# Optimization experiments

Hardware: AMD Instinct MI355X
Metric: run time of the kernel (lower is better)

The kernel has to match this reference:

```python
import jax, jax.numpy as jnp
import numpy as np

CAM_FL = 540.0
CAM_W, CAM_H = 640, 480
FILTER_STD = 1.0
FILTER_SCALE = 1.0
RADIUS = int(np.ceil(2.0 * FILTER_STD))  # truncate Gaussian footprint at 2 std
K = 2 * RADIUS + 1                        # 5x5 footprint


def setup_inputs() -> dict:
    key = jax.random.key(0)
    k1, k2, k3, k4 = jax.random.split(key, 4)
    B, N = 4, 200000
    locs = jax.random.normal(k1, (B, N, 3), jnp.float32) * 2.0
    camera_pose = jax.random.normal(k2, (B, 3), jnp.float32) * 0.1
    camera_rot = jax.random.normal(k3, (B, 4), jnp.float32)
    # depth in [0, 10): some particles occluded, some visible
    depth_mask = jax.random.uniform(k4, (B, CAM_H, CAM_W), jnp.float32) * 10.0
    return {"locs": locs, "camera_pose": camera_pose,
            "camera_rot": camera_rot, "depth_mask": depth_mask}


def _rot_from_quat(q):
    # Matches torch _rotationMatrixFromQuaternion layout: R[b, i, j]
    qx, qy, qz, qw = q[:, 0], q[:, 1], q[:, 2], q[:, 3]
    qx2, qy2, qz2 = qx * qx, qy * qy, qz * qz
    qxqy, qxqz, qxqw = qx * qy, qx * qz, qx * qw
    qyqz, qyqw, qzqw = qy * qz, qy * qw, qz * qw
    r00 = 1 - 2 * qy2 - 2 * qz2
    r10 = 2 * qxqy - 2 * qzqw
    r20 = 2 * qxqz + 2 * qyqw
    r01 = 2 * qxqy + 2 * qzqw
    r11 = 1 - 2 * qx2 - 2 * qz2
    r21 = 2 * qyqz - 2 * qxqw
    r02 = 2 * qxqz - 2 * qyqw
    r12 = 2 * qyqz + 2 * qxqw
    r22 = 1 - 2 * qx2 - 2 * qy2
    row0 = jnp.stack([r00, r01, r02], axis=-1)
    row1 = jnp.stack([r10, r11, r12], axis=-1)
    row2 = jnp.stack([r20, r21, r22], axis=-1)
    return jnp.stack([row0, row1, row2], axis=-2)  # (B,3,3)


def reference(locs, camera_pose, camera_rot, depth_mask):
    B, N, _ = locs.shape
    # transform into camera frame
    p = locs - camera_pose[:, None, :]
    q = camera_rot / jnp.sqrt(jnp.sum(camera_rot ** 2, axis=1, keepdims=True))
    q = q * jnp.array([-1.0, -1.0, -1.0, 1.0], q.dtype)  # conjugate -> inverse rotation
    R = jax.lax.stop_gradient(_rot_from_quat(q))          # torch uses quat.data (detached)
    p = jnp.einsum('bni,bij->bnj', p, R)                  # torch.bmm(locs, rot)
    x, y, z = p[..., 0], p[..., 1], p[..., 2]
    zsafe = jnp.where(z > 0, z, 1.0)
    # pinhole projection, principal point at image center
    px = x / zsafe * CAM_FL + CAM_W / 2.0   # (B,N)
    py = y / zsafe * CAM_FL + CAM_H / 2.0
    offs = jnp.arange(K, dtype=jnp.int32) - RADIUS
    jx = jnp.floor(px).astype(jnp.int32)[..., None] + offs   # (B,N,K) column idx
    iy = jnp.floor(py).astype(jnp.int32)[..., None] + offs   # (B,N,K) row idx
    dx = jx.astype(px.dtype) - px[..., None]
    dy = iy.astype(py.dtype) - py[..., None]
    # (B,N,K,K) Gaussian footprint weights
    w = FILTER_SCALE * jnp.exp(-(dy[..., :, None] ** 2 + dx[..., None, :] ** 2)
                               / (2.0 * FILTER_STD ** 2))
    ii = jnp.broadcast_to(iy[..., :, None], w.shape)
    jj = jnp.broadcast_to(jx[..., None, :], w.shape)
    inb = (ii >= 0) & (ii < CAM_H) & (jj >= 0) & (jj < CAM_W)
    iic = jnp.clip(ii, 0, CAM_H - 1)
    jjc = jnp.clip(jj, 0, CAM_W - 1)
    bidx = jnp.arange(B, dtype=jnp.int32)[:, None, None, None]
    d = depth_mask[bidx, iic, jjc]          # per-pixel occlusion depth
    zb = z[..., None, None]
    valid = inb & (zb > 0) & (zb <= d)      # in front of camera and not occluded
    w = jnp.where(valid, w, 0.0)
    out = jnp.zeros((B, CAM_H, CAM_W), locs.dtype)
    out = out.at[bidx, iic, jjc].add(w)
    return out
```

## Files before the change

### kernel.cpp

```cpp
#include <hip/hip_runtime.h>

#define CAM_FL 540.0f
#define CAM_W  640
#define CAM_H  480
#define RADIUS 2
#define KSIZE  (2 * RADIUS + 1)
#define TAPS   (KSIZE * KSIZE)
#define BLK    256

__global__ __launch_bounds__(BLK) void particle_project_kernel(
    const float* __restrict__ locs,
    const float* __restrict__ camera_pose,
    const float* __restrict__ camera_rot,
    const float* __restrict__ depth,
    float* __restrict__ out,
    int N)
{
#pragma clang fp contract(off)
    __shared__ int   s_iy0[BLK];
    __shared__ int   s_jx0[BLK];
    __shared__ float s_z[BLK];
    __shared__ float s_wy[BLK][KSIZE];
    __shared__ float s_wx[BLK][KSIZE];
    __shared__ int   s_cnt;

    const int b   = blockIdx.y;
    const int n   = blockIdx.x * blockDim.x + threadIdx.x;
    const int tid = threadIdx.x;

    if (tid == 0) s_cnt = 0;

    const float qx_raw = camera_rot[b * 4 + 0];
    const float qy_raw = camera_rot[b * 4 + 1];
    const float qz_raw = camera_rot[b * 4 + 2];
    const float qw_raw = camera_rot[b * 4 + 3];
    const float norm2 = ((qx_raw * qx_raw + qy_raw * qy_raw) + qz_raw * qz_raw) + qw_raw * qw_raw;
    const float s = sqrtf(norm2);
    const float qx = -(qx_raw / s);
    const float qy = -(qy_raw / s);
    const float qz = -(qz_raw / s);
    const float qw =  (qw_raw / s);

    const float qx2 = qx * qx, qy2 = qy * qy, qz2 = qz * qz;
    const float qxqy = qx * qy, qxqz = qx * qz, qxqw = qx * qw;
    const float qyqz = qy * qz, qyqw = qy * qw, qzqw = qz * qw;
    const float r00 = (1.0f - 2.0f * qy2) - 2.0f * qz2;
    const float r10 = 2.0f * qxqy - 2.0f * qzqw;
    const float r20 = 2.0f * qxqz + 2.0f * qyqw;
    const float r01 = 2.0f * qxqy + 2.0f * qzqw;
    const float r11 = (1.0f - 2.0f * qx2) - 2.0f * qz2;
    const float r21 = 2.0f * qyqz - 2.0f * qxqw;
    const float r02 = 2.0f * qxqz - 2.0f * qyqw;
    const float r12 = 2.0f * qyqz + 2.0f * qxqw;
    const float r22 = (1.0f - 2.0f * qx2) - 2.0f * qy2;

    const float cpx = camera_pose[b * 3 + 0];
    const float cpy = camera_pose[b * 3 + 1];
    const float cpz = camera_pose[b * 3 + 2];

    bool alive = (n < N);
    float px = 0.0f, py = 0.0f, z = 0.0f;
    if (alive) {
        const float p0 = locs[(size_t)(b * N + n) * 3 + 0] - cpx;
        const float p1 = locs[(size_t)(b * N + n) * 3 + 1] - cpy;
        const float p2 = locs[(size_t)(b * N + n) * 3 + 2] - cpz;

        const float x = (p0 * r00 + p1 * r10) + p2 * r20;
        const float y = (p0 * r01 + p1 * r11) + p2 * r21;
        z             = (p0 * r02 + p1 * r12) + p2 * r22;

        alive = (z > 0.0f);
        if (alive) {
            px = (x / z) * CAM_FL + (float)CAM_W * 0.5f;
            py = (y / z) * CAM_FL + (float)CAM_H * 0.5f;
            alive = (px >= -(float)RADIUS && px < (float)(CAM_W + RADIUS) &&
                     py >= -(float)RADIUS && py < (float)(CAM_H + RADIUS));
        }
    }

    __syncthreads();

    const unsigned long long mask = __ballot(alive);
    const int lane   = tid & 63;
    const int rank   = __popcll(mask & ((1ull << lane) - 1ull));
    const int wcount = __popcll(mask);

    int wbase_v = 0;
    if (lane == 0 && wcount > 0) wbase_v = atomicAdd(&s_cnt, wcount);
    const int wbase = __shfl(wbase_v, 0);

    if (alive) {
        const int i   = wbase + rank;
        const int iy0 = (int)floorf(py);
        const int jx0 = (int)floorf(px);
        s_iy0[i] = iy0;
        s_jx0[i] = jx0;
        s_z[i]   = z;
#pragma unroll
        for (int k = 0; k < KSIZE; ++k) {
            const float dyf = (float)(iy0 + k - RADIUS) - py;
            const float dxf = (float)(jx0 + k - RADIUS) - px;
            s_wy[i][k] = __expf(-(dyf * dyf) * 0.5f);
            s_wx[i][k] = __expf(-(dxf * dxf) * 0.5f);
        }
    }

    __syncthreads();

    const int ns    = s_cnt;
    const int total = ns * TAPS;
    const float* depth_b = depth + (size_t)b * (CAM_H * CAM_W);
    float*       out_b   = out   + (size_t)b * (CAM_H * CAM_W);

    for (int t = tid; t < total; t += BLK) {
        const int si  = t / TAPS;
        const int tap = t - si * TAPS;
        const int ti  = tap / KSIZE;
        const int tj  = tap - ti * KSIZE;

        const int iy = s_iy0[si] + ti - RADIUS;
        const int jx = s_jx0[si] + tj - RADIUS;
        if ((unsigned)iy >= (unsigned)CAM_H || (unsigned)jx >= (unsigned)CAM_W)
            continue;

        const int pix = iy * CAM_W + jx;
        const float d = depth_b[pix];
        if (s_z[si] <= d) {
            const float w = s_wy[si][ti] * s_wx[si][tj];
            atomicAdd(&out_b[pix], w);
        }
    }
}

extern "C" void kernel_launch(void* const* d_in, const int* in_sizes, int n_in,
                              void* d_out, int out_size, void* d_ws, size_t ws_size,
                              hipStream_t stream) {
    const float* locs        = (const float*)d_in[0];
    const float* camera_pose = (const float*)d_in[1];
    const float* camera_rot  = (const float*)d_in[2];
    const float* depth_mask  = (const float*)d_in[3];
    float* out = (float*)d_out;

    const int B = in_sizes[1] / 3;
    const int N = in_sizes[0] / (3 * B);

    hipMemsetAsync(d_out, 0, (size_t)out_size * sizeof(float), stream);

    dim3 block(BLK, 1, 1);
    dim3 grid((N + BLK - 1) / BLK, B, 1);
    particle_project_kernel<<<grid, block, 0, stream>>>(
        locs, camera_pose, camera_rot, depth_mask, out, N);
}
```

Baseline: 86.89 us.

## Stage locs via vector loads, swizzle block-to-batch mapping, batch depth gathers

Particle coordinates are now loaded cooperatively into shared memory with 16-byte nontemporal vector loads instead of strided 12-byte per-thread loads. A 1D grid with a swizzle for B=4 interleaves batches across consecutive blocks, likely to spread atomics and depth reads across the four images and XCDs. The splat loop processes two taps per iteration so the depth loads are issued before the atomics. This adds shared memory and a specialized mapping path that only applies when B is 4 and the chunk count is even.

After: 88.63 us. About the same (+2.0%).

```diff
diff --git a/kernel.cpp b/kernel.cpp
--- a/kernel.cpp
+++ b/kernel.cpp
@@ -8,15 +8,18 @@
 #define TAPS   (KSIZE * KSIZE)
 #define BLK    256
 
+typedef float floatx4 __attribute__((ext_vector_type(4)));
+
 __global__ __launch_bounds__(BLK) void particle_project_kernel(
     const float* __restrict__ locs,
     const float* __restrict__ camera_pose,
     const float* __restrict__ camera_rot,
     const float* __restrict__ depth,
     float* __restrict__ out,
-    int N)
+    int N, int chunks, int swiz)
 {
 #pragma clang fp contract(off)
+    __shared__ float s_loc[BLK * 3];
     __shared__ int   s_iy0[BLK];
     __shared__ int   s_jx0[BLK];
     __shared__ float s_z[BLK];
@@ -24,11 +27,31 @@
     __shared__ float s_wx[BLK][KSIZE];
     __shared__ int   s_cnt;
 
-    const int b   = blockIdx.y;
-    const int n   = blockIdx.x * blockDim.x + threadIdx.x;
     const int tid = threadIdx.x;
+    const int bid = blockIdx.x;
+
+    int b, chunk;
+    if (swiz) { b = (bid & 7) >> 1; chunk = ((bid >> 3) << 1) | (bid & 1); }
+    else      { b = bid / chunks;   chunk = bid - b * chunks; }
+
+    const int n0   = chunk * BLK;
+    const int nrem = min(BLK, N - n0);
 
     if (tid == 0) s_cnt = 0;
+
+    {
+        const float* src = locs + ((size_t)b * N + (size_t)n0) * 3;
+        const int remf = nrem * 3;
+        const int nv4  = remf >> 2;
+        const floatx4* src4 = (const floatx4*)src;
+        for (int i = tid; i < nv4; i += BLK) {
+            const floatx4 v = __builtin_nontemporal_load(src4 + i);
+            s_loc[i * 4 + 0] = v.x; s_loc[i * 4 + 1] = v.y;
+            s_loc[i * 4 + 2] = v.z; s_loc[i * 4 + 3] = v.w;
+        }
+        for (int i = (nv4 << 2) + tid; i < remf; i += BLK)
+            s_loc[i] = src[i];
+    }
 
     const float qx_raw = camera_rot[b * 4 + 0];
     const float qy_raw = camera_rot[b * 4 + 1];
@@ -58,12 +81,14 @@
     const float cpy = camera_pose[b * 3 + 1];
     const float cpz = camera_pose[b * 3 + 2];
 
-    bool alive = (n < N);
+    __syncthreads();
+
+    bool alive = (tid < nrem);
     float px = 0.0f, py = 0.0f, z = 0.0f;
     if (alive) {
-        const float p0 = locs[(size_t)(b * N + n) * 3 + 0] - cpx;
-        const float p1 = locs[(size_t)(b * N + n) * 3 + 1] - cpy;
-        const float p2 = locs[(size_t)(b * N + n) * 3 + 2] - cpz;
+        const float p0 = s_loc[tid * 3 + 0] - cpx;
+        const float p1 = s_loc[tid * 3 + 1] - cpy;
+        const float p2 = s_loc[tid * 3 + 2] - cpz;
 
         const float x = (p0 * r00 + p1 * r10) + p2 * r20;
         const float y = (p0 * r01 + p1 * r11) + p2 * r21;
@@ -77,8 +102,6 @@
                      py >= -(float)RADIUS && py < (float)(CAM_H + RADIUS));
         }
     }
-
-    __syncthreads();
 
     const unsigned long long mask = __ballot(alive);
     const int lane   = tid & 63;
@@ -112,23 +135,33 @@
     const float* depth_b = depth + (size_t)b * (CAM_H * CAM_W);
     float*       out_b   = out   + (size_t)b * (CAM_H * CAM_W);
 
-    for (int t = tid; t < total; t += BLK) {
-        const int si  = t / TAPS;
-        const int tap = t - si * TAPS;
-        const int ti  = tap / KSIZE;
-        const int tj  = tap - ti * KSIZE;
-
-        const int iy = s_iy0[si] + ti - RADIUS;
-        const int jx = s_jx0[si] + tj - RADIUS;
-        if ((unsigned)iy >= (unsigned)CAM_H || (unsigned)jx >= (unsigned)CAM_W)
-            continue;
-
-        const int pix = iy * CAM_W + jx;
-        const float d = depth_b[pix];
-        if (s_z[si] <= d) {
-            const float w = s_wy[si][ti] * s_wx[si][tj];
-            atomicAdd(&out_b[pix], w);
+    for (int t0 = tid; t0 < total; t0 += 2 * BLK) {
+        int   pixA[2];
+        float zA[2], wA[2], dA[2];
+        bool  okA[2];
+#pragma unroll
+        for (int u = 0; u < 2; ++u) {
+            const int t = t0 + u * BLK;
+            bool ok = (t < total);
+            int si = 0, tap = 0;
+            if (ok) { si = t / TAPS; tap = t - si * TAPS; }
+            const int ti = tap / KSIZE;
+            const int tj = tap - ti * KSIZE;
+            const int iy = s_iy0[si] + ti - RADIUS;
+            const int jx = s_jx0[si] + tj - RADIUS;
+            ok = ok && ((unsigned)iy < (unsigned)CAM_H) && ((unsigned)jx < (unsigned)CAM_W);
+            pixA[u] = iy * CAM_W + jx;
+            zA[u]   = s_z[si];
+            wA[u]   = s_wy[si][ti] * s_wx[si][tj];
+            okA[u]  = ok;
+            dA[u]   = 0.0f;
         }
+#pragma unroll
+        for (int u = 0; u < 2; ++u)
+            if (okA[u]) dA[u] = depth_b[pixA[u]];
+#pragma unroll
+        for (int u = 0; u < 2; ++u)
+            if (okA[u] && zA[u] <= dA[u]) atomicAdd(&out_b[pixA[u]], wA[u]);
     }
 }
 
@@ -143,11 +176,13 @@
 
     const int B = in_sizes[1] / 3;
     const int N = in_sizes[0] / (3 * B);
+    const int chunks = (N + BLK - 1) / BLK;
+    const int swiz = (B == 4 && (chunks % 2) == 0) ? 1 : 0;
 
-    hipMemsetAsync(d_out, 0, (size_t)out_size * sizeof(float), stream);
+    (void)hipMemsetAsync(d_out, 0, (size_t)out_size * sizeof(float), stream);
 
     dim3 block(BLK, 1, 1);
-    dim3 grid((N + BLK - 1) / BLK, B, 1);
+    dim3 grid(B * chunks, 1, 1);
     particle_project_kernel<<<grid, block, 0, stream>>>(
-        locs, camera_pose, camera_rot, depth_mask, out, N);
+        locs, camera_pose, camera_rot, depth_mask, out, N, chunks, swiz);
 }
```

## Fuse output zeroing into persistent cooperative kernel with grid sync

Applied to the files above, without the earlier changes.

Replaces the separate memset and one-block-per-chunk launch with a single cooperative persistent kernel of fixed grid size. The kernel zeroes the output with vector stores, synchronizes the whole grid, then loops over particle chunks. Each chunk's locations are staged through shared memory with vectorized loads. This removes a separate launch and makes the location loads coalesced, at the cost of a grid-wide barrier, a fixed grid that may not fully occupy the device, and extra per-chunk block barriers.

After: 158.2 us. +82.1%, slower.

```diff
diff --git a/kernel.cpp b/kernel.cpp
--- a/kernel.cpp
+++ b/kernel.cpp
@@ -1,4 +1,7 @@
 #include <hip/hip_runtime.h>
+#include <hip/hip_cooperative_groups.h>
+
+namespace cg = cooperative_groups;
 
 #define CAM_FL 540.0f
 #define CAM_W  640
@@ -7,6 +10,9 @@
 #define KSIZE  (2 * RADIUS + 1)
 #define TAPS   (KSIZE * KSIZE)
 #define BLK    256
+#define GRID   1024
+
+typedef float floatx4 __attribute__((ext_vector_type(4)));
 
 __global__ __launch_bounds__(BLK) void particle_project_kernel(
     const float* __restrict__ locs,
@@ -14,9 +20,10 @@
     const float* __restrict__ camera_rot,
     const float* __restrict__ depth,
     float* __restrict__ out,
-    int N)
+    int N, int chunksPerB, int B, int out_elems)
 {
 #pragma clang fp contract(off)
+    __shared__ float s_loc[BLK * 3];
     __shared__ int   s_iy0[BLK];
     __shared__ int   s_jx0[BLK];
     __shared__ float s_z[BLK];
@@ -24,111 +31,144 @@
     __shared__ float s_wx[BLK][KSIZE];
     __shared__ int   s_cnt;
 
-    const int b   = blockIdx.y;
-    const int n   = blockIdx.x * blockDim.x + threadIdx.x;
-    const int tid = threadIdx.x;
+    const int tid   = threadIdx.x;
+    const int gtid  = blockIdx.x * BLK + tid;
+    const int gsize = gridDim.x * BLK;
 
-    if (tid == 0) s_cnt = 0;
+    {
+        const int nv4 = out_elems >> 2;
+        floatx4* out4 = (floatx4*)out;
+        const floatx4 z4 = {0.0f, 0.0f, 0.0f, 0.0f};
+        for (int i = gtid; i < nv4; i += gsize) out4[i] = z4;
+        for (int i = (nv4 << 2) + gtid; i < out_elems; i += gsize) out[i] = 0.0f;
+    }
+    cg::this_grid().sync();
 
-    const float qx_raw = camera_rot[b * 4 + 0];
-    const float qy_raw = camera_rot[b * 4 + 1];
-    const float qz_raw = camera_rot[b * 4 + 2];
-    const float qw_raw = camera_rot[b * 4 + 3];
-    const float norm2 = ((qx_raw * qx_raw + qy_raw * qy_raw) + qz_raw * qz_raw) + qw_raw * qw_raw;
-    const float s = sqrtf(norm2);
-    const float qx = -(qx_raw / s);
-    const float qy = -(qy_raw / s);
-    const float qz = -(qz_raw / s);
-    const float qw =  (qw_raw / s);
+    const int totalChunks = B * chunksPerB;
+    for (int c = blockIdx.x; c < totalChunks; c += gridDim.x) {
+        const int b     = c / chunksPerB;
+        const int chunk = c - b * chunksPerB;
+        const int n0    = chunk * BLK;
+        const int nrem  = min(BLK, N - n0);
 
-    const float qx2 = qx * qx, qy2 = qy * qy, qz2 = qz * qz;
-    const float qxqy = qx * qy, qxqz = qx * qz, qxqw = qx * qw;
-    const float qyqz = qy * qz, qyqw = qy * qw, qzqw = qz * qw;
-    const float r00 = (1.0f - 2.0f * qy2) - 2.0f * qz2;
-    const float r10 = 2.0f * qxqy - 2.0f * qzqw;
-    const float r20 = 2.0f * qxqz + 2.0f * qyqw;
-    const float r01 = 2.0f * qxqy + 2.0f * qzqw;
-    const float r11 = (1.0f - 2.0f * qx2) - 2.0f * qz2;
-    const float r21 = 2.0f * qyqz - 2.0f * qxqw;
-    const float r02 = 2.0f * qxqz - 2.0f * qyqw;
-    const float r12 = 2.0f * qyqz + 2.0f * qxqw;
-    const float r22 = (1.0f - 2.0f * qx2) - 2.0f * qy2;
+        if (tid == 0) s_cnt = 0;
 
-    const float cpx = camera_pose[b * 3 + 0];
-    const float cpy = camera_pose[b * 3 + 1];
-    const float cpz = camera_pose[b * 3 + 2];
+        {
+            const float* src = locs + ((size_t)b * N + (size_t)n0) * 3;
+            const int remf = nrem * 3;
+            const int nv4  = remf >> 2;
+            const floatx4* src4 = (const floatx4*)src;
+            for (int i = tid; i < nv4; i += BLK) {
+                const floatx4 v = src4[i];
+                s_loc[i * 4 + 0] = v.x; s_loc[i * 4 + 1] = v.y;
+                s_loc[i * 4 + 2] = v.z; s_loc[i * 4 + 3] = v.w;
+            }
+            for (int i = (nv4 << 2) + tid; i < remf; i += BLK)
+                s_loc[i] = src[i];
+        }
 
-    bool alive = (n < N);
-    float px = 0.0f, py = 0.0f, z = 0.0f;
-    if (alive) {
-        const float p0 = locs[(size_t)(b * N + n) * 3 + 0] - cpx;
-        const float p1 = locs[(size_t)(b * N + n) * 3 + 1] - cpy;
-        const float p2 = locs[(size_t)(b * N + n) * 3 + 2] - cpz;
+        const float qx_raw = camera_rot[b * 4 + 0];
+        const float qy_raw = camera_rot[b * 4 + 1];
+        const float qz_raw = camera_rot[b * 4 + 2];
+        const float qw_raw = camera_rot[b * 4 + 3];
+        const float norm2 = ((qx_raw * qx_raw + qy_raw * qy_raw) + qz_raw * qz_raw) + qw_raw * qw_raw;
+        const float s = sqrtf(norm2);
+        const float qx = -(qx_raw / s);
+        const float qy = -(qy_raw / s);
+        const float qz = -(qz_raw / s);
+        const float qw =  (qw_raw / s);
 
-        const float x = (p0 * r00 + p1 * r10) + p2 * r20;
-        const float y = (p0 * r01 + p1 * r11) + p2 * r21;
-        z             = (p0 * r02 + p1 * r12) + p2 * r22;
+        const float qx2 = qx * qx, qy2 = qy * qy, qz2 = qz * qz;
+        const float qxqy = qx * qy, qxqz = qx * qz, qxqw = qx * qw;
+        const float qyqz = qy * qz, qyqw = qy * qw, qzqw = qz * qw;
+        const float r00 = (1.0f - 2.0f * qy2) - 2.0f * qz2;
+        const float r10 = 2.0f * qxqy - 2.0f * qzqw;
+        const float r20 = 2.0f * qxqz + 2.0f * qyqw;
+        const float r01 = 2.0f * qxqy + 2.0f * qzqw;
+        const float r11 = (1.0f - 2.0f * qx2) - 2.0f * qz2;
+        const float r21 = 2.0f * qyqz - 2.0f * qxqw;
+        const float r02 = 2.0f * qxqz - 2.0f * qyqw;
+        const float r12 = 2.0f * qyqz + 2.0f * qxqw;
+        const float r22 = (1.0f - 2.0f * qx2) - 2.0f * qy2;
 
-        alive = (z > 0.0f);
+        const float cpx = camera_pose[b * 3 + 0];
+        const float cpy = camera_pose[b * 3 + 1];
+        const float cpz = camera_pose[b * 3 + 2];
+
+        __syncthreads();
+
+        bool alive = (tid < nrem);
+        float px = 0.0f, py = 0.0f, z = 0.0f;
         if (alive) {
-            px = (x / z) * CAM_FL + (float)CAM_W * 0.5f;
-            py = (y / z) * CAM_FL + (float)CAM_H * 0.5f;
-            alive = (px >= -(float)RADIUS && px < (float)(CAM_W + RADIUS) &&
-                     py >= -(float)RADIUS && py < (float)(CAM_H + RADIUS));
+            const float p0 = s_loc[tid * 3 + 0] - cpx;
+            const float p1 = s_loc[tid * 3 + 1] - cpy;
+            const float p2 = s_loc[tid * 3 + 2] - cpz;
+
+            const float x = (p0 * r00 + p1 * r10) + p2 * r20;
+            const float y = (p0 * r01 + p1 * r11) + p2 * r21;
+            z             = (p0 * r02 + p1 * r12) + p2 * r22;
+
+            alive = (z > 0.0f);
+            if (alive) {
+                px = (x / z) * CAM_FL + (float)CAM_W * 0.5f;
+                py = (y / z) * CAM_FL + (float)CAM_H * 0.5f;
+                alive = (px >= -(float)RADIUS && px < (float)(CAM_W + RADIUS) &&
+                         py >= -(float)RADIUS && py < (float)(CAM_H + RADIUS));
+            }
         }
-    }
 
-    __syncthreads();
+        const unsigned long long mask = __ballot(alive);
+        const int lane   = tid & 63;
+        const int rank   = __popcll(mask & ((1ull << lane) - 1ull));
+        const int wcount = __popcll(mask);
 
-    const unsigned long long mask = __ballot(alive);
-    const int lane   = tid & 63;
-    const int rank   = __popcll(mask & ((1ull << lane) - 1ull));
-    const int wcount = __popcll(mask);
+        int wbase_v = 0;
+        if (lane == 0 && wcount > 0) wbase_v = atomicAdd(&s_cnt, wcount);
+        const int wbase = __shfl(wbase_v, 0);
 
-    int wbase_v = 0;
-    if (lane == 0 && wcount > 0) wbase_v = atomicAdd(&s_cnt, wcount);
-    const int wbase = __shfl(wbase_v, 0);
+        if (alive) {
+            const int i   = wbase + rank;
+            const int iy0 = (int)floorf(py);
+            const int jx0 = (int)floorf(px);
+            s_iy0[i] = iy0;
+            s_jx0[i] = jx0;
+            s_z[i]   = z;
+#pragma unroll
+            for (int k = 0; k < KSIZE; ++k) {
+                const float dyf = (float)(iy0 + k - RADIUS) - py;
+                const float dxf = (float)(jx0 + k - RADIUS) - px;
+                s_wy[i][k] = __expf(-(dyf * dyf) * 0.5f);
+                s_wx[i][k] = __expf(-(dxf * dxf) * 0.5f);
+            }
+        }
 
-    if (alive) {
-        const int i   = wbase + rank;
-        const int iy0 = (int)floorf(py);
-        const int jx0 = (int)floorf(px);
-        s_iy0[i] = iy0;
-        s_jx0[i] = jx0;
-        s_z[i]   = z;
-#pragma unroll
-        for (int k = 0; k < KSIZE; ++k) {
-            const float dyf = (float)(iy0 + k - RADIUS) - py;
-            const float dxf = (float)(jx0 + k - RADIUS) - px;
-            s_wy[i][k] = __expf(-(dyf * dyf) * 0.5f);
-            s_wx[i][k] = __expf(-(dxf * dxf) * 0.5f);
+        __syncthreads();
+
+        const int ns    = s_cnt;
+        const int total = ns * TAPS;
+        const float* depth_b = depth + (size_t)b * (CAM_H * CAM_W);
+        float*       out_b   = out   + (size_t)b * (CAM_H * CAM_W);
+
+        for (int t = tid; t < total; t += BLK) {
+            const int si  = t / TAPS;
+            const int tap = t - si * TAPS;
+            const int ti  = tap / KSIZE;
+            const int tj  = tap - ti * KSIZE;
+
+            const int iy = s_iy0[si] + ti - RADIUS;
+            const int jx = s_jx0[si] + tj - RADIUS;
+            if ((unsigned)iy >= (unsigned)CAM_H || (unsigned)jx >= (unsigned)CAM_W)
+                continue;
+
+            const int pix = iy * CAM_W + jx;
+            const float d = depth_b[pix];
+            if (s_z[si] <= d) {
+                const float w = s_wy[si][ti] * s_wx[si][tj];
+                atomicAdd(&out_b[pix], w);
+            }
         }
-    }
 
-    __syncthreads();
-
-    const int ns    = s_cnt;
-    const int total = ns * TAPS;
-    const float* depth_b = depth + (size_t)b * (CAM_H * CAM_W);
-    float*       out_b   = out   + (size_t)b * (CAM_H * CAM_W);
-
-    for (int t = tid; t < total; t += BLK) {
-        const int si  = t / TAPS;
-        const int tap = t - si * TAPS;
-        const int ti  = tap / KSIZE;
-        const int tj  = tap - ti * KSIZE;
-
-        const int iy = s_iy0[si] + ti - RADIUS;
-        const int jx = s_jx0[si] + tj - RADIUS;
-        if ((unsigned)iy >= (unsigned)CAM_H || (unsigned)jx >= (unsigned)CAM_W)
-            continue;
-
-        const int pix = iy * CAM_W + jx;
-        const float d = depth_b[pix];
-        if (s_z[si] <= d) {
-            const float w = s_wy[si][ti] * s_wx[si][tj];
-            atomicAdd(&out_b[pix], w);
-        }
+        __syncthreads();
     }
 }
 
@@ -141,13 +181,16 @@
     const float* depth_mask  = (const float*)d_in[3];
     float* out = (float*)d_out;
 
-    const int B = in_sizes[1] / 3;
-    const int N = in_sizes[0] / (3 * B);
+    int B = in_sizes[1] / 3;
+    int N = in_sizes[0] / (3 * B);
+    int chunksPerB = (N + BLK - 1) / BLK;
+    int out_elems = out_size;
 
-    hipMemsetAsync(d_out, 0, (size_t)out_size * sizeof(float), stream);
-
-    dim3 block(BLK, 1, 1);
-    dim3 grid((N + BLK - 1) / BLK, B, 1);
-    particle_project_kernel<<<grid, block, 0, stream>>>(
-        locs, camera_pose, camera_rot, depth_mask, out, N);
+    void* args[] = {
+        (void*)&locs, (void*)&camera_pose, (void*)&camera_rot, (void*)&depth_mask,
+        (void*)&out, (void*)&N, (void*)&chunksPerB, (void*)&B, (void*)&out_elems
+    };
+    (void)hipLaunchCooperativeKernel((void*)particle_project_kernel,
+                                     dim3(GRID, 1, 1), dim3(BLK, 1, 1),
+                                     args, 0, stream);
 }
```
